# Kernel tuning notes

Hardware: AMD Instinct MI355X
Metric: run time of the kernel (lower is better)

## Reference

```python
import jax, jax.numpy as jnp
import numpy as np

EPS = 1e-5  # torch BatchNorm1d default eps


def setup_inputs() -> dict:
    key = jax.random.key(0)
    ks = jax.random.split(key, 8)
    F, P = 32, 64            # frames, peds per frame
    B = F * P                # batch = 2048
    E, H, M, D = 64, 128, 512, 1024  # embed, h_dim, pool_mlp_dim, bottleneck
    starts = np.arange(F, dtype=np.int64) * P
    seq_start_end = jnp.asarray(np.stack([starts, starts + P], axis=1))
    inp = {
        "curr_h_states": jax.random.normal(ks[0], (1, B, H), dtype=jnp.float32),
        "curr_pos": jax.random.normal(ks[1], (B, 2), dtype=jnp.float32),
        "seq_start_end": seq_start_end,
        # embedding: Linear(2, E)
        "We": jax.random.normal(ks[2], (2, E), dtype=jnp.float32) * 0.5,
        "be": jnp.zeros((E,), dtype=jnp.float32),
        # mlp layer 1: Linear(E+H, M) + BN(M)
        "W1": jax.random.normal(ks[3], (E + H, M), dtype=jnp.float32) * 0.05,
        "b1": jnp.zeros((M,), dtype=jnp.float32),
        "g1": jnp.ones((M,), dtype=jnp.float32),
        "beta1": jnp.zeros((M,), dtype=jnp.float32),
        # mlp layer 2: Linear(M, D) + BN(D)
        "W2": jax.random.normal(ks[4], (M, D), dtype=jnp.float32) * 0.04,
        "b2": jnp.zeros((D,), dtype=jnp.float32),
        "g2": jnp.ones((D,), dtype=jnp.float32),
        "beta2": jnp.zeros((D,), dtype=jnp.float32),
        # BN running stats (eval mode)
        "rm1": jnp.zeros((M,), dtype=jnp.float32),
        "rv1": jnp.ones((M,), dtype=jnp.float32),
        "rm2": jnp.zeros((D,), dtype=jnp.float32),
        "rv2": jnp.ones((D,), dtype=jnp.float32),
    }
    return inp


def _bn(x, g, beta, rm, rv):
    return g * (x - rm) * jax.lax.rsqrt(rv + EPS) + beta


def reference(curr_h_states, curr_pos, seq_start_end, We, be, W1, b1, g1, beta1,
              W2, b2, g2, beta2, rm1, rv1, rm2, rv2):
    # Equal-size frames: vectorize the per-frame Python loop via a reshape.
    F = seq_start_end.shape[0]
    B = curr_h_states.shape[1]
    P = B // F
    h = curr_h_states[0].reshape(F, P, -1)      # (F, P, H)
    pos = curr_pos.reshape(F, P, 2)             # (F, P, 2)
    # rel_pos[f, i, j] = pos[f, j] - pos[f, i]  (repeat minus repeat_interleave)
    rel = pos[:, None, :, :] - pos[:, :, None, :]          # (F, P, P, 2)
    emb = rel @ We + be                                     # (F, P, P, E)
    h_rep = jnp.broadcast_to(h[:, None, :, :], (F, P, P, h.shape[-1]))
    x = jnp.concatenate([emb, h_rep], axis=-1)              # (F, P, P, E+H)
    x = jax.nn.relu(_bn(x @ W1 + b1, g1, beta1, rm1, rv1))  # (F, P, P, M)
    x = jax.nn.relu(_bn(x @ W2 + b2, g2, beta2, rm2, rv2))  # (F, P, P, D)
    pool_h = x.max(axis=2)                                  # max over j -> (F, P, D)
    return pool_h.reshape(B, -1)                            # (B, D)
```

## Files before the change

kernel.cpp:

```cpp
#include <hip/hip_runtime.h>
#include <hip/hip_bf16.h>
#include <stdint.h>

#define EPS_BN 1e-5f

constexpr int Fn = 32;
constexpr int Pn = 64;
constexpr int Bn = 2048;
constexpr int Hn = 128;
constexpr int En = 64;
constexpr int Mn = 512;
constexpr int Dn = 1024;

using bf16x8 = __attribute__((ext_vector_type(8))) short;
using f32x4  = __attribute__((ext_vector_type(4))) float;

static __device__ __forceinline__ float    bcf(uint32_t u) { return __builtin_bit_cast(float, u); }
static __device__ __forceinline__ uint32_t bcu(float f)    { return __builtin_bit_cast(uint32_t, f); }
static __device__ __forceinline__ unsigned short bfbits(float f) {
  return __builtin_bit_cast(unsigned short, __float2bfloat16(f));
}

static __device__ __forceinline__ void dma16(const uint4* g, uint4* l) {
  __builtin_amdgcn_global_load_lds(
      (const __attribute__((address_space(1))) unsigned int*)g,
      (__attribute__((address_space(3))) unsigned int*)l, 16, 0, 0);
}

static __device__ __forceinline__ bf16x8 mk_af(uint4 a, uint4 q) {
  uint4 x;
#pragma unroll
  for (int v = 0; v < 4; ++v) {
    uint32_t aw = ((const uint32_t*)&a)[v], qw = ((const uint32_t*)&q)[v];
    float lo = fmaxf(bcf(aw << 16) - bcf(qw << 16), 0.f);
    float hi = fmaxf(bcf(aw) - bcf(qw), 0.f);
    ((uint32_t*)&x)[v] = __builtin_amdgcn_perm(bcu(hi), bcu(lo), 0x07060302u);
  }
  return __builtin_bit_cast(bf16x8, x);
}

__global__ void prep_all(const float* __restrict__ hs, const float* __restrict__ pos,
                         const float* __restrict__ We, const float* __restrict__ be,
                         const float* __restrict__ W1, const float* __restrict__ b1,
                         const float* __restrict__ g1, const float* __restrict__ beta1,
                         const float* __restrict__ rm1, const float* __restrict__ rv1,
                         const float* __restrict__ W2, const float* __restrict__ b2,
                         const float* __restrict__ g2, const float* __restrict__ beta2,
                         const float* __restrict__ rm2, const float* __restrict__ rv2,
                         __hip_bfloat16* __restrict__ Agb, __hip_bfloat16* __restrict__ Qgb,
                         uint4* __restrict__ W2f, float* __restrict__ c2) {
  __shared__ float smem[64 * 65];
  int bid = blockIdx.x, t = threadIdx.x;
  if (bid < 256) {
    int rb = bid * 8, m = t;
    float* hsh = smem;
    float* psh = smem + 1024;
    for (int idx = t; idx < 8 * Hn; idx += 512) hsh[idx] = hs[rb * Hn + idx];
    if (t < 16) psh[t] = pos[rb * 2 + t];
    __syncthreads();
    float w0 = 0.f, w1 = 0.f, c = 0.f;
    for (int e = 0; e < En; ++e) {
      float w = W1[e * Mn + m];
      w0 += We[e] * w; w1 += We[En + e] * w; c += be[e] * w;
    }
    c += b1[m];
    float s  = g1[m] * rsqrtf(rv1[m] + EPS_BN);
    float tt = beta1[m] - rm1[m] * s;
    float acc[8];
#pragma unroll
    for (int ri = 0; ri < 8; ++ri) acc[ri] = c;
    for (int e = 0; e < Hn; ++e) {
      float w = W1[(En + e) * Mn + m];
#pragma unroll
      for (int ri = 0; ri < 8; ++ri) acc[ri] += hsh[ri * Hn + e] * w;
    }
#pragma unroll
    for (int ri = 0; ri < 8; ++ri) {
      float q = psh[ri * 2] * w0 + psh[ri * 2 + 1] * w1;
      Agb[(rb + ri) * Mn + m] = __float2bfloat16((acc[ri] + q) * s + tt);
      Qgb[(rb + ri) * Mn + m] = __float2bfloat16(q * s);
    }
  } else {
    int b2i = bid - 256;
    int d0 = (b2i & 15) * 64, k0 = (b2i >> 4) * 64;
    int col = t & 63, row8 = t >> 6;
#pragma unroll
    for (int rr = 0; rr < 8; ++rr) {
      int row = rr * 8 + row8;
      smem[row * 65 + col] = W2[(k0 + row) * Dn + d0 + col];
    }
    __syncthreads();
    int lane = t & 63, q8 = t >> 6;
    int sel = q8 & 3, kcl = q8 >> 2;
    int dl = sel * 16 + (lane & 15), d = d0 + dl;
    float sf = g2[d] * rsqrtf(rv2[d] + EPS_BN);
    int kb = kcl * 32 + (lane >> 4) * 8;
    uint32_t wd[4];
#pragma unroll
    for (int h = 0; h < 4; ++h) {
      uint32_t u0 = bfbits(smem[(kb + 2 * h) * 65 + dl] * sf);
      uint32_t u1 = bfbits(smem[(kb + 2 * h + 1) * 65 + dl] * sf);
      wd[h] = u0 | (u1 << 16);
    }
    int ntile = (d0 >> 4) + sel;
    int kc    = (k0 >> 5) + kcl;
    W2f[(ntile * 16 + kc) * 64 + lane] = (uint4){wd[0], wd[1], wd[2], wd[3]};
    if (k0 == 0 && t < 64) {
      int dd = d0 + t;
      float ss = g2[dd] * rsqrtf(rv2[dd] + EPS_BN);
      c2[dd] = b2[dd] * ss + beta2[dd] - rm2[dd] * ss;
    }
  }
}

__launch_bounds__(256, 2)
__global__ void gemm_pool(const __hip_bfloat16* __restrict__ Agb,
                          const __hip_bfloat16* __restrict__ Qgb,
                          const uint4* __restrict__ W2f,
                          const float* __restrict__ c2, float* __restrict__ out) {
  __shared__ uint4 Bs[4096];

  int ct = blockIdx.x;
  int rt = blockIdx.y;
  int f = rt >> 4, i0 = (rt & 15) * 4;

  int t = threadIdx.x, lane = t & 63, w = t >> 6;
  int jw = w & 1, dw = w >> 1;
  int dw4 = dw * 4;

  int jr0 = 32 * jw + (lane & 15);
  int ko  = (lane >> 4) * 8;

  const uint4* aP0 = (const uint4*)(Agb + (f * Pn + jr0) * Mn + ko);
  const uint4* aP1 = (const uint4*)(Agb + (f * Pn + jr0 + 16) * Mn + ko);
  const uint4* qP0 = (const uint4*)(Qgb + (f * Pn + i0 + 0) * Mn + ko);
  const uint4* qP1 = (const uint4*)(Qgb + (f * Pn + i0 + 1) * Mn + ko);
  const uint4* qP2 = (const uint4*)(Qgb + (f * Pn + i0 + 2) * Mn + ko);
  const uint4* qP3 = (const uint4*)(Qgb + (f * Pn + i0 + 3) * Mn + ko);
  const uint4* W2base = W2f + (size_t)(ct * 8) * 16 * 64 + lane;

  f32x4 acc[4][2][4];
#pragma unroll
  for (int i = 0; i < 4; ++i)
#pragma unroll
    for (int mt = 0; mt < 2; ++mt)
#pragma unroll
      for (int nt = 0; nt < 4; ++nt) acc[i][mt][nt] = (f32x4){0.f, 0.f, 0.f, 0.f};

  uint4 rA0 = aP0[0], rA1 = aP1[0];
  uint4 rQ0 = qP0[0], rQ1 = qP1[0], rQ2 = qP2[0], rQ3 = qP3[0];

  for (int ph = 0; ph < 2; ++ph) {
    if (ph) __syncthreads();
#pragma unroll
    for (int s = 0; s < 16; ++s) {
      int idx = w * 16 + s;
      int kc8 = idx >> 3, gnt = idx & 7;
      dma16(W2base + (gnt * 16 + ph * 8 + kc8) * 64, Bs + idx * 64);
    }
    __syncthreads();

    for (int kc8 = 0; kc8 < 8; ++kc8) {
      int kc = ph * 8 + kc8;
      bf16x8 bg[4];
#pragma unroll
      for (int nt = 0; nt < 4; ++nt)
        bg[nt] = *(const bf16x8*)(Bs + (kc8 * 8 + dw4 + nt) * 64 + lane);

      int kn = (kc < 15) ? kc + 1 : 15;
      uint4 nA0 = aP0[kn * 4], nA1 = aP1[kn * 4];
      uint4 nQ0 = qP0[kn * 4], nQ1 = qP1[kn * 4];
      uint4 nQ2 = qP2[kn * 4], nQ3 = qP3[kn * 4];

#pragma unroll
      for (int i = 0; i < 4; ++i) {
        uint4 q = (i == 0) ? rQ0 : (i == 1) ? rQ1 : (i == 2) ? rQ2 : rQ3;
        bf16x8 af0 = mk_af(rA0, q);
        bf16x8 af1 = mk_af(rA1, q);
#pragma unroll
        for (int nt = 0; nt < 4; ++nt) {
          acc[i][0][nt] = __builtin_amdgcn_mfma_f32_16x16x32_bf16(af0, bg[nt], acc[i][0][nt], 0, 0, 0);
          acc[i][1][nt] = __builtin_amdgcn_mfma_f32_16x16x32_bf16(af1, bg[nt], acc[i][1][nt], 0, 0, 0);
        }
      }
      rA0 = nA0; rA1 = nA1;
      rQ0 = nQ0; rQ1 = nQ1; rQ2 = nQ2; rQ3 = nQ3;
    }
  }

  __syncthreads();
  float* redf = (float*)Bs;
#pragma unroll
  for (int i = 0; i < 4; ++i) {
#pragma unroll
    for (int nt = 0; nt < 4; ++nt) {
      f32x4 a0 = acc[i][0][nt], a1 = acc[i][1][nt];
      float mx = fmaxf(fmaxf(fmaxf(a0[0], a0[1]), fmaxf(a0[2], a0[3])),
                       fmaxf(fmaxf(a1[0], a1[1]), fmaxf(a1[2], a1[3])));
      mx = fmaxf(mx, __shfl_xor(mx, 16));
      mx = fmaxf(mx, __shfl_xor(mx, 32));
      if (lane < 16) redf[(jw * 4 + i) * 128 + dw * 64 + nt * 16 + lane] = mx;
    }
  }
  __syncthreads();
#pragma unroll
  for (int r = t; r < 512; r += 256) {
    int i = r >> 7, d = r & 127;
    float v = fmaxf(redf[i * 128 + d], redf[(4 + i) * 128 + d]);
    out[(f * Pn + i0 + i) * Dn + ct * 128 + d] = fmaxf(v + c2[ct * 128 + d], 0.f);
  }
}

extern "C" void kernel_launch(void* const* d_in, const int* in_sizes, int n_in,
                              void* d_out, int out_size, void* d_ws, size_t ws_size,
                              hipStream_t stream) {
  const float* hs    = (const float*)d_in[0];
  const float* pos   = (const float*)d_in[1];
  const float* We    = (const float*)d_in[3];
  const float* be    = (const float*)d_in[4];
  const float* W1    = (const float*)d_in[5];
  const float* b1    = (const float*)d_in[6];
  const float* g1    = (const float*)d_in[7];
  const float* beta1 = (const float*)d_in[8];
  const float* W2    = (const float*)d_in[9];
  const float* b2    = (const float*)d_in[10];
  const float* g2    = (const float*)d_in[11];
  const float* beta2 = (const float*)d_in[12];
  const float* rm1   = (const float*)d_in[13];
  const float* rv1   = (const float*)d_in[14];
  const float* rm2   = (const float*)d_in[15];
  const float* rv2   = (const float*)d_in[16];

  char* ws = (char*)d_ws;
  float* c2 = (float*)(ws + 0);
  __hip_bfloat16* Agb = (__hip_bfloat16*)(ws + 4096);
  __hip_bfloat16* Qgb = (__hip_bfloat16*)(ws + 4096 + 2097152);
  uint4* W2f = (uint4*)(ws + 4096 + 2 * 2097152);
  float* out = (float*)d_out;

  prep_all<<<384, 512, 0, stream>>>(hs, pos, We, be, W1, b1, g1, beta1, rm1, rv1,
                                    W2, b2, g2, beta2, rm2, rv2, Agb, Qgb, W2f, c2);
  gemm_pool<<<dim3(Dn / 128, (Fn * Pn * Pn) / 256), 256, 0, stream>>>(Agb, Qgb, W2f, c2, out);
}
```

Before: 268.5 us.

## Switch pooled GEMM to 32x32x16 MFMA with per-wave row ownership

The main GEMM moves from 16x16x32 to 32x32x16 bf16 MFMA tiles. Each wave now owns one query row i and all 64 j rows across 128 output columns, so the max-pool reduction stays inside the wave and no longer goes through LDS. W2 is repacked in the prep kernel to match the new fragment layout. The prep kernel also uses 4 rows per block instead of 8, doubling its block count. Each A fragment built by mk_af now feeds more MFMAs, which cuts elementwise prep work per FLOP, but each wave holds 128 accumulator registers.

```diff
diff --git a/kernel.cpp b/kernel.cpp
--- a/kernel.cpp
+++ b/kernel.cpp
@@ -12,8 +12,8 @@
 constexpr int Mn = 512;
 constexpr int Dn = 1024;
 
-using bf16x8 = __attribute__((ext_vector_type(8))) short;
-using f32x4  = __attribute__((ext_vector_type(4))) float;
+using bf16x8  = __attribute__((ext_vector_type(8))) short;
+using f32x16  = __attribute__((ext_vector_type(16))) float;
 
 static __device__ __forceinline__ float    bcf(uint32_t u) { return __builtin_bit_cast(float, u); }
 static __device__ __forceinline__ uint32_t bcu(float f)    { return __builtin_bit_cast(uint32_t, f); }
@@ -48,15 +48,15 @@
                          const float* __restrict__ g2, const float* __restrict__ beta2,
                          const float* __restrict__ rm2, const float* __restrict__ rv2,
                          __hip_bfloat16* __restrict__ Agb, __hip_bfloat16* __restrict__ Qgb,
-                         uint4* __restrict__ W2f, float* __restrict__ c2) {
+                         uint4* __restrict__ W2g, float* __restrict__ c2) {
   __shared__ float smem[64 * 65];
   int bid = blockIdx.x, t = threadIdx.x;
-  if (bid < 256) {
-    int rb = bid * 8, m = t;
+  if (bid < 512) {
+    int rb = bid * 4, m = t;
     float* hsh = smem;
-    float* psh = smem + 1024;
-    for (int idx = t; idx < 8 * Hn; idx += 512) hsh[idx] = hs[rb * Hn + idx];
-    if (t < 16) psh[t] = pos[rb * 2 + t];
+    float* psh = smem + 512;
+    if (t < 4 * Hn) hsh[t] = hs[rb * Hn + t];
+    if (t < 8) psh[t] = pos[rb * 2 + t];
     __syncthreads();
     float w0 = 0.f, w1 = 0.f, c = 0.f;
     for (int e = 0; e < En; ++e) {
@@ -66,22 +66,22 @@
     c += b1[m];
     float s  = g1[m] * rsqrtf(rv1[m] + EPS_BN);
     float tt = beta1[m] - rm1[m] * s;
-    float acc[8];
-#pragma unroll
-    for (int ri = 0; ri < 8; ++ri) acc[ri] = c;
+    float acc[4];
+#pragma unroll
+    for (int ri = 0; ri < 4; ++ri) acc[ri] = c;
     for (int e = 0; e < Hn; ++e) {
       float w = W1[(En + e) * Mn + m];
 #pragma unroll
-      for (int ri = 0; ri < 8; ++ri) acc[ri] += hsh[ri * Hn + e] * w;
-    }
-#pragma unroll
-    for (int ri = 0; ri < 8; ++ri) {
+      for (int ri = 0; ri < 4; ++ri) acc[ri] += hsh[ri * Hn + e] * w;
+    }
+#pragma unroll
+    for (int ri = 0; ri < 4; ++ri) {
       float q = psh[ri * 2] * w0 + psh[ri * 2 + 1] * w1;
       Agb[(rb + ri) * Mn + m] = __float2bfloat16((acc[ri] + q) * s + tt);
       Qgb[(rb + ri) * Mn + m] = __float2bfloat16(q * s);
     }
   } else {
-    int b2i = bid - 256;
+    int b2i = bid - 512;
     int d0 = (b2i & 15) * 64, k0 = (b2i >> 4) * 64;
     int col = t & 63, row8 = t >> 6;
 #pragma unroll
@@ -91,10 +91,10 @@
     }
     __syncthreads();
     int lane = t & 63, q8 = t >> 6;
-    int sel = q8 & 3, kcl = q8 >> 2;
-    int dl = sel * 16 + (lane & 15), d = d0 + dl;
+    int sel_n = q8 & 1, sel_ks = q8 >> 1;
+    int dl = sel_n * 32 + (lane & 31), d = d0 + dl;
     float sf = g2[d] * rsqrtf(rv2[d] + EPS_BN);
-    int kb = kcl * 32 + (lane >> 4) * 8;
+    int kb = sel_ks * 16 + (lane >> 5) * 8;
     uint32_t wd[4];
 #pragma unroll
     for (int h = 0; h < 4; ++h) {
@@ -102,9 +102,9 @@
       uint32_t u1 = bfbits(smem[(kb + 2 * h + 1) * 65 + dl] * sf);
       wd[h] = u0 | (u1 << 16);
     }
-    int ntile = (d0 >> 4) + sel;
-    int kc    = (k0 >> 5) + kcl;
-    W2f[(ntile * 16 + kc) * 64 + lane] = (uint4){wd[0], wd[1], wd[2], wd[3]};
+    int n32 = (d0 >> 5) + sel_n;
+    int ks  = (k0 >> 4) + sel_ks;
+    W2g[(n32 * 32 + ks) * 64 + lane] = (uint4){wd[0], wd[1], wd[2], wd[3]};
     if (k0 == 0 && t < 64) {
       int dd = d0 + t;
       float ss = g2[dd] * rsqrtf(rv2[dd] + EPS_BN);
@@ -116,7 +116,7 @@
 __launch_bounds__(256, 2)
 __global__ void gemm_pool(const __hip_bfloat16* __restrict__ Agb,
                           const __hip_bfloat16* __restrict__ Qgb,
-                          const uint4* __restrict__ W2f,
+                          const uint4* __restrict__ W2g,
                           const float* __restrict__ c2, float* __restrict__ out) {
   __shared__ uint4 Bs[4096];
 
@@ -125,89 +125,75 @@
   int f = rt >> 4, i0 = (rt & 15) * 4;
 
   int t = threadIdx.x, lane = t & 63, w = t >> 6;
-  int jw = w & 1, dw = w >> 1;
-  int dw4 = dw * 4;
-
-  int jr0 = 32 * jw + (lane & 15);
-  int ko  = (lane >> 4) * 8;
-
-  const uint4* aP0 = (const uint4*)(Agb + (f * Pn + jr0) * Mn + ko);
-  const uint4* aP1 = (const uint4*)(Agb + (f * Pn + jr0 + 16) * Mn + ko);
-  const uint4* qP0 = (const uint4*)(Qgb + (f * Pn + i0 + 0) * Mn + ko);
-  const uint4* qP1 = (const uint4*)(Qgb + (f * Pn + i0 + 1) * Mn + ko);
-  const uint4* qP2 = (const uint4*)(Qgb + (f * Pn + i0 + 2) * Mn + ko);
-  const uint4* qP3 = (const uint4*)(Qgb + (f * Pn + i0 + 3) * Mn + ko);
-  const uint4* W2base = W2f + (size_t)(ct * 8) * 16 * 64 + lane;
-
-  f32x4 acc[4][2][4];
-#pragma unroll
-  for (int i = 0; i < 4; ++i)
-#pragma unroll
-    for (int mt = 0; mt < 2; ++mt)
-#pragma unroll
-      for (int nt = 0; nt < 4; ++nt) acc[i][mt][nt] = (f32x4){0.f, 0.f, 0.f, 0.f};
-
-  uint4 rA0 = aP0[0], rA1 = aP1[0];
-  uint4 rQ0 = qP0[0], rQ1 = qP1[0], rQ2 = qP2[0], rQ3 = qP3[0];
+  int i = i0 + w;
+  int ko = lane >> 5;
+
+  const uint4* aPj0 = (const uint4*)(Agb + (f * Pn + (lane & 31)) * Mn) + ko;
+  const uint4* aPj1 = (const uint4*)(Agb + (f * Pn + 32 + (lane & 31)) * Mn) + ko;
+  const uint4* qP   = (const uint4*)(Qgb + (f * Pn + i) * Mn) + ko;
+  const uint4* W2base = W2g + (size_t)(4 * ct) * 32 * 64 + lane;
+
+  f32x16 acc[2][4];
+#pragma unroll
+  for (int jf = 0; jf < 2; ++jf)
+#pragma unroll
+    for (int nf = 0; nf < 4; ++nf)
+      acc[jf][nf] = (f32x16){0.f,0.f,0.f,0.f,0.f,0.f,0.f,0.f,0.f,0.f,0.f,0.f,0.f,0.f,0.f,0.f};
+
+  uint4 rA00 = aPj0[0], rA01 = aPj1[0], rQ0 = qP[0];
+  uint4 rA10 = aPj0[2], rA11 = aPj1[2], rQ1 = qP[2];
 
   for (int ph = 0; ph < 2; ++ph) {
     if (ph) __syncthreads();
 #pragma unroll
     for (int s = 0; s < 16; ++s) {
-      int idx = w * 16 + s;
-      int kc8 = idx >> 3, gnt = idx & 7;
-      dma16(W2base + (gnt * 16 + ph * 8 + kc8) * 64, Bs + idx * 64);
+      int slot = w * 16 + s;
+      int ksl = slot >> 2, nf = slot & 3;
+      dma16(W2base + (nf * 32 + ph * 16 + ksl) * 64, Bs + slot * 64);
     }
     __syncthreads();
 
     for (int kc8 = 0; kc8 < 8; ++kc8) {
       int kc = ph * 8 + kc8;
-      bf16x8 bg[4];
-#pragma unroll
-      for (int nt = 0; nt < 4; ++nt)
-        bg[nt] = *(const bf16x8*)(Bs + (kc8 * 8 + dw4 + nt) * 64 + lane);
-
       int kn = (kc < 15) ? kc + 1 : 15;
-      uint4 nA0 = aP0[kn * 4], nA1 = aP1[kn * 4];
-      uint4 nQ0 = qP0[kn * 4], nQ1 = qP1[kn * 4];
-      uint4 nQ2 = qP2[kn * 4], nQ3 = qP3[kn * 4];
-
-#pragma unroll
-      for (int i = 0; i < 4; ++i) {
-        uint4 q = (i == 0) ? rQ0 : (i == 1) ? rQ1 : (i == 2) ? rQ2 : rQ3;
-        bf16x8 af0 = mk_af(rA0, q);
-        bf16x8 af1 = mk_af(rA1, q);
-#pragma unroll
-        for (int nt = 0; nt < 4; ++nt) {
-          acc[i][0][nt] = __builtin_amdgcn_mfma_f32_16x16x32_bf16(af0, bg[nt], acc[i][0][nt], 0, 0, 0);
-          acc[i][1][nt] = __builtin_amdgcn_mfma_f32_16x16x32_bf16(af1, bg[nt], acc[i][1][nt], 0, 0, 0);
+      {
+        bf16x8 af0 = mk_af(rA00, rQ0);
+        bf16x8 af1 = mk_af(rA01, rQ0);
+#pragma unroll
+        for (int nf = 0; nf < 4; ++nf) {
+          bf16x8 bg = *(const bf16x8*)(Bs + ((kc8 * 2 + 0) * 4 + nf) * 64 + lane);
+          acc[0][nf] = __builtin_amdgcn_mfma_f32_32x32x16_bf16(af0, bg, acc[0][nf], 0, 0, 0);
+          acc[1][nf] = __builtin_amdgcn_mfma_f32_32x32x16_bf16(af1, bg, acc[1][nf], 0, 0, 0);
         }
       }
-      rA0 = nA0; rA1 = nA1;
-      rQ0 = nQ0; rQ1 = nQ1; rQ2 = nQ2; rQ3 = nQ3;
-    }
-  }
-
-  __syncthreads();
-  float* redf = (float*)Bs;
-#pragma unroll
-  for (int i = 0; i < 4; ++i) {
-#pragma unroll
-    for (int nt = 0; nt < 4; ++nt) {
-      f32x4 a0 = acc[i][0][nt], a1 = acc[i][1][nt];
-      float mx = fmaxf(fmaxf(fmaxf(a0[0], a0[1]), fmaxf(a0[2], a0[3])),
-                       fmaxf(fmaxf(a1[0], a1[1]), fmaxf(a1[2], a1[3])));
-      mx = fmaxf(mx, __shfl_xor(mx, 16));
-      mx = fmaxf(mx, __shfl_xor(mx, 32));
-      if (lane < 16) redf[(jw * 4 + i) * 128 + dw * 64 + nt * 16 + lane] = mx;
-    }
-  }
-  __syncthreads();
-#pragma unroll
-  for (int r = t; r < 512; r += 256) {
-    int i = r >> 7, d = r & 127;
-    float v = fmaxf(redf[i * 128 + d], redf[(4 + i) * 128 + d]);
-    out[(f * Pn + i0 + i) * Dn + ct * 128 + d] = fmaxf(v + c2[ct * 128 + d], 0.f);
+      rA00 = aPj0[kn * 4]; rA01 = aPj1[kn * 4]; rQ0 = qP[kn * 4];
+      {
+        bf16x8 af0 = mk_af(rA10, rQ1);
+        bf16x8 af1 = mk_af(rA11, rQ1);
+#pragma unroll
+        for (int nf = 0; nf < 4; ++nf) {
+          bf16x8 bg = *(const bf16x8*)(Bs + ((kc8 * 2 + 1) * 4 + nf) * 64 + lane);
+          acc[0][nf] = __builtin_amdgcn_mfma_f32_32x32x16_bf16(af0, bg, acc[0][nf], 0, 0, 0);
+          acc[1][nf] = __builtin_amdgcn_mfma_f32_32x32x16_bf16(af1, bg, acc[1][nf], 0, 0, 0);
+        }
+      }
+      rA10 = aPj0[kn * 4 + 2]; rA11 = aPj1[kn * 4 + 2]; rQ1 = qP[kn * 4 + 2];
+    }
+  }
+
+#pragma unroll
+  for (int nf = 0; nf < 4; ++nf) {
+    float mx = 0.f;
+#pragma unroll
+    for (int jf = 0; jf < 2; ++jf)
+#pragma unroll
+      for (int rg = 0; rg < 16; ++rg)
+        mx = fmaxf(mx, acc[jf][nf][rg]);
+    mx = fmaxf(mx, __shfl_xor(mx, 32));
+    if (lane < 32) {
+      int d = ct * 128 + nf * 32 + (lane & 31);
+      out[(f * Pn + i) * Dn + d] = fmaxf(mx + c2[d], 0.f);
+    }
   }
 }
 
@@ -235,10 +221,10 @@
   float* c2 = (float*)(ws + 0);
   __hip_bfloat16* Agb = (__hip_bfloat16*)(ws + 4096);
   __hip_bfloat16* Qgb = (__hip_bfloat16*)(ws + 4096 + 2097152);
-  uint4* W2f = (uint4*)(ws + 4096 + 2 * 2097152);
+  uint4* W2g = (uint4*)(ws + 4096 + 2 * 2097152);
   float* out = (float*)d_out;
 
-  prep_all<<<384, 512, 0, stream>>>(hs, pos, We, be, W1, b1, g1, beta1, rm1, rv1,
-                                    W2, b2, g2, beta2, rm2, rv2, Agb, Qgb, W2f, c2);
-  gemm_pool<<<dim3(Dn / 128, (Fn * Pn * Pn) / 256), 256, 0, stream>>>(Agb, Qgb, W2f, c2, out);
-}
+  prep_all<<<640, 512, 0, stream>>>(hs, pos, We, be, W1, b1, g1, beta1, rm1, rv1,
+                                    W2, b2, g2, beta2, rm2, rv2, Agb, Qgb, W2g, c2);
+  gemm_pool<<<dim3(Dn / 128, (Fn * Pn * Pn) / 256), 256, 0, stream>>>(Agb, Qgb, W2g, c2, out);
+}
```

Result: no change. 264.6 us (-1.5%).
